# Optimization experiments

Measured on AMD Instinct MI355X. Metric: run time of the kernel, lower is better.

## Reference

```python
import jax, jax.numpy as jnp
import numpy as np

NUM_HEADS = 16

def setup_inputs() -> dict:
    key = jax.random.key(0)
    ks = jax.random.split(key, 5)
    B, T, C = 2, 2048, 1024
    s = 0.02
    return {
        "x": jax.random.normal(ks[0], (B, T, C), dtype=jnp.float32),
        "attn_w": jax.random.normal(ks[1], (3 * C, C), dtype=jnp.float32) * s,
        "attn_b": jax.random.normal(ks[2], (3 * C,), dtype=jnp.float32) * s,
        "proj_w": jax.random.normal(ks[3], (C, C), dtype=jnp.float32) * s,
        "proj_b": jax.random.normal(ks[4], (C,), dtype=jnp.float32) * s,
    }

def reference(x, attn_w, attn_b, proj_w, proj_b):
    B, T, C = x.shape
    H = NUM_HEADS
    D = C // H
    # fused QKV projection (torch Linear: x @ W^T + b)
    qkv = x @ attn_w.T + attn_b                      # [B, T, 3C]
    q, k, v = jnp.split(qkv, 3, axis=-1)             # each [B, T, C]
    # split heads -> [B, H, T, D]
    def heads(t):
        return t.reshape(B, T, H, D).transpose(0, 2, 1, 3)
    q, k, v = heads(q), heads(k), heads(v)
    scale = 1.0 / jnp.sqrt(jnp.asarray(D, dtype=x.dtype))
    scores = jnp.einsum("bhtd,bhsd->bhts", q, k) * scale   # [B, H, T, T]
    causal = jnp.tril(jnp.ones((T, T), dtype=bool))
    scores = jnp.where(causal[None, None], scores, jnp.asarray(-jnp.inf, dtype=scores.dtype))
    att = jax.nn.softmax(scores, axis=-1)
    out = jnp.einsum("bhts,bhsd->bhtd", att, v)      # [B, H, T, D]
    out = out.transpose(0, 2, 1, 3).reshape(B, T, C)
    return out @ proj_w.T + proj_b
```

## Files before the change

kernel.cpp:

```cpp
#include <hip/hip_runtime.h>
#include <hip/hip_bf16.h>

typedef __bf16 bf16_t;
typedef __bf16 bf16x4 __attribute__((ext_vector_type(4)));
typedef __bf16 bf16x8 __attribute__((ext_vector_type(8)));
typedef float f32x4 __attribute__((ext_vector_type(4)));
typedef float f32x8 __attribute__((ext_vector_type(8)));

#define MFMA16(a, b, c) __builtin_amdgcn_mfma_f32_16x16x32_bf16(a, b, c, 0, 0, 0)

#define GLOAD_LDS16(g, l)                                              \
  __builtin_amdgcn_global_load_lds(                                    \
      (const __attribute__((address_space(1))) unsigned int*)(g),      \
      (__attribute__((address_space(3))) unsigned int*)(l), 16, 0, 0)

constexpr int B = 2, T = 2048, C = 1024, H = 16, D = 64;
constexpr int NQKV = 3 * C;
constexpr int M = B * T;

__global__ __launch_bounds__(256) void cvt_kernel(
    const float* __restrict__ s0, bf16_t* __restrict__ d0, int n0,
    const float* __restrict__ s1, bf16_t* __restrict__ d1, int n1,
    const float* __restrict__ s2, bf16_t* __restrict__ d2, int n2)
{
  const float* s; bf16_t* d; int n;
  if (blockIdx.y == 0)      { s = s0; d = d0; n = n0; }
  else if (blockIdx.y == 1) { s = s1; d = d1; n = n1; }
  else                      { s = s2; d = d2; n = n2; }
  const int idx = (blockIdx.x * 256 + threadIdx.x) * 8;
  if (idx >= n) return;
  f32x8 t = *(const f32x8*)(s + idx);
  bf16x8 r;
#pragma unroll
  for (int j = 0; j < 8; ++j) r[j] = (bf16_t)t[j];
  *(bf16x8*)(d + idx) = r;
}

template<int BN, int NI>
__device__ __forceinline__ void gemm_mainloop_db(
    const bf16_t* __restrict__ A, const bf16_t* __restrict__ Wt,
    const int K, const int m0, const int n0,
    bf16_t* ldsA0, bf16_t* ldsA1, bf16_t* ldsB0, bf16_t* ldsB1,
    f32x4 acc[4][NI])
{
  const int tid  = threadIdx.x;
  const int wv   = tid >> 6;
  const int lane = tid & 63;
  const int col  = lane & 15;
  const int quad = lane >> 4;
  const int lr8  = lane >> 3;
  const int cpos = lane & 7;
  const int wm = wv >> 1, wn = wv & 1;
  constexpr int BJ = BN / 32;
  constexpr int BRW = BN / 4;

  const bf16_t* ag[4]; const bf16_t* bg[BJ];
#pragma unroll
  for (int j = 0; j < 4; ++j)
    ag[j] = A + (size_t)(m0 + wv * 32 + j * 8 + lr8) * K + (cpos ^ lr8) * 8;
#pragma unroll
  for (int j = 0; j < BJ; ++j)
    bg[j] = Wt + (size_t)(n0 + wv * BRW + j * 8 + lr8) * K + (cpos ^ lr8) * 8;

  const int xa = quad ^ (col & 7);
  const int niter = K / 64;

#pragma unroll
  for (int j = 0; j < 4; ++j)
    GLOAD_LDS16(ag[j], ldsA0 + (wv * 32 + j * 8) * 64);
#pragma unroll
  for (int j = 0; j < BJ; ++j)
    GLOAD_LDS16(bg[j], ldsB0 + (wv * BRW + j * 8) * 64);

  for (int it = 0; it < niter; ++it) {
    __syncthreads();
    const bf16_t* cA = (it & 1) ? ldsA1 : ldsA0;
    const bf16_t* cB = (it & 1) ? ldsB1 : ldsB0;
    if (it + 1 < niter) {
      bf16_t* nA = (it & 1) ? ldsA0 : ldsA1;
      bf16_t* nB = (it & 1) ? ldsB0 : ldsB1;
      const int off = (it + 1) * 64;
#pragma unroll
      for (int j = 0; j < 4; ++j)
        GLOAD_LDS16(ag[j] + off, nA + (wv * 32 + j * 8) * 64);
#pragma unroll
      for (int j = 0; j < BJ; ++j)
        GLOAD_LDS16(bg[j] + off, nB + (wv * BRW + j * 8) * 64);
    }
#pragma unroll
    for (int ks = 0; ks < 2; ++ks) {
      const int xk = (xa ^ (ks * 4)) * 8;
      bf16x8 af[4], bfr[NI];
#pragma unroll
      for (int mi = 0; mi < 4; ++mi)
        af[mi] = *(const bf16x8*)(cA + (wm * 64 + mi * 16 + col) * 64 + xk);
#pragma unroll
      for (int ni = 0; ni < NI; ++ni)
        bfr[ni] = *(const bf16x8*)(cB + (wn * (NI * 16) + ni * 16 + col) * 64 + xk);
#pragma unroll
      for (int mi = 0; mi < 4; ++mi)
#pragma unroll
        for (int ni = 0; ni < NI; ++ni)
          acc[mi][ni] = MFMA16(af[mi], bfr[ni], acc[mi][ni]);
    }
  }
}

__global__ __launch_bounds__(256) void qkv_gemm_kernel(
    const bf16_t* __restrict__ x, const bf16_t* __restrict__ w,
    const float* __restrict__ bias,
    bf16_t* __restrict__ qws, bf16_t* __restrict__ kws, bf16_t* __restrict__ vws)
{
  __shared__ __align__(16) bf16_t ldsA[2][128 * 64];
  __shared__ __align__(16) bf16_t ldsB[2][128 * 64];
  const int lane = threadIdx.x & 63;
  const int wv   = threadIdx.x >> 6;
  const int col  = lane & 15;
  const int quad = lane >> 4;
  const int wm = wv >> 1, wn = wv & 1;
  const int m0 = blockIdx.y * 128;
  const int n0 = blockIdx.x * 128;

  f32x4 acc[4][4] = {};
  gemm_mainloop_db<128, 4>(x, w, C, m0, n0,
                           ldsA[0], ldsA[1], ldsB[0], ldsB[1], acc);

  const int which = n0 >> 10;

  if (which == 2) {
    __syncthreads();
    bf16_t* vt = &ldsA[0][0] + wv * 4096;

#pragma unroll
    for (int ni = 0; ni < 4; ++ni) {
      const int n = n0 + wn * 64 + ni * 16 + col;
      const float bval = bias[n];
      const int d = n & 63;
#pragma unroll
      for (int r = 0; r < 4; ++r) {
        bf16x4 pw;
#pragma unroll
        for (int mi = 0; mi < 4; ++mi)
          pw[mi] = (bf16_t)(acc[mi][ni][r] + bval);
        const int k = 2 * quad + (r >> 1);
        const int S = d * 8 + (k ^ (d & 7));
        *(bf16x4*)(vt + S * 8 + (r & 1) * 4) = pw;
      }
    }

    const int b   = (m0 + wm * 64) >> 11;
    const int t0w = (m0 + wm * 64) & (T - 1);
    const int h   = ((n0 & (C - 1)) + wn * 64) >> 6;
    const size_t bh = (size_t)(b * H + h);
    const int lr8 = lane >> 3;
    const int c8  = lane & 7;
#pragma unroll
    for (int j = 0; j < 8; ++j) {
      const int d = j * 8 + lr8;
      bf16x8 row = *(const bf16x8*)(vt + (d * 8 + (c8 ^ (d & 7))) * 8);
      *(bf16x8*)(vws + (bh * D + d) * T + t0w + c8 * 8) = row;
    }
  } else {
#pragma unroll
    for (int ni = 0; ni < 4; ++ni) {
      const int n = n0 + wn * 64 + ni * 16 + col;
      const float bval = bias[n];
      const int c = n & (C - 1);
      const int h = c >> 6;
      const int d = c & 63;
#pragma unroll
      for (int mi = 0; mi < 4; ++mi) {
#pragma unroll
        for (int r = 0; r < 4; ++r) {
          const int m = m0 + wm * 64 + mi * 16 + quad * 4 + r;
          const int b = m >> 11;
          const int t = m & (T - 1);
          const bf16_t bv = (bf16_t)(acc[mi][ni][r] + bval);
          const size_t bh = (size_t)(b * H + h);
          if (which == 0) qws[(bh * T + t) * D + d] = bv;
          else            kws[(bh * T + t) * D + d] = bv;
        }
      }
    }
  }
}

__global__ __launch_bounds__(256) void attn_kernel(
    const bf16_t* __restrict__ qws, const bf16_t* __restrict__ kws,
    const bf16_t* __restrict__ vws, bf16_t* __restrict__ yws)
{
  const int bh = blockIdx.y;
  const int tid  = threadIdx.x;
  const int wv   = tid >> 6;
  const int lane = tid & 63;
  const int col  = lane & 15;
  const int quad = lane >> 4;

  const bf16_t* Q  = qws + (size_t)bh * T * D;
  const bf16_t* K  = kws + (size_t)bh * T * D;
  const bf16_t* Vt = vws + (size_t)bh * D * T;

  __shared__ __align__(16) bf16_t ldsK[2][64 * 64];
  __shared__ __align__(16) bf16_t ldsV[2][64 * 64];
  __shared__ __align__(16) bf16_t ldsP[4][16 * 64];
  bf16_t* ldsPw = ldsP[wv];

  const float cscale = 0.125f * 1.44269504088896340736f;

  const int xs   = col & 7;
  const int cxq  = (quad ^ xs) * 8;
  const int lr8  = lane >> 3;
  const int ksrc = (lane & 7) ^ lr8;
  const int pxor = (quad & 1) * 4;
  const int b = bh >> 4;
  const int h = bh & 15;

#pragma unroll
  for (int half = 0; half < 2; ++half) {
    const int qt = half == 0 ? (31 - (int)blockIdx.x) : (int)blockIdx.x;
    const int t0 = qt * 64;
    const int tw = t0 + 16 * wv;
    const int niter = qt + 1;

    bf16x8 qf0 = *(const bf16x8*)(Q + (size_t)(tw + col) * D + quad * 8);
    bf16x8 qf1 = *(const bf16x8*)(Q + (size_t)(tw + col) * D + 32 + quad * 8);

    f32x4 o[4] = {};
    f32x4 lp = {};

    __syncthreads();

#pragma unroll
    for (int j = 0; j < 2; ++j) {
      GLOAD_LDS16(K + (size_t)(16 * wv + j * 8 + lr8) * D + ksrc * 8,
                  ldsK[0] + (16 * wv + j * 8) * 64);
      GLOAD_LDS16(Vt + (size_t)(16 * wv + j * 8 + lr8) * T + ksrc * 8,
                  ldsV[0] + (16 * wv + j * 8) * 64);
    }

    for (int it = 0; it < niter; ++it) {
      const int s0 = it * 64;
      __syncthreads();

      if (it + 1 < niter) {
        const int sn = s0 + 64;
        bf16_t* dK = ldsK[(it + 1) & 1];
        bf16_t* dV = ldsV[(it + 1) & 1];
#pragma unroll
        for (int j = 0; j < 2; ++j) {
          GLOAD_LDS16(K + (size_t)(sn + 16 * wv + j * 8 + lr8) * D + ksrc * 8,
                      dK + (16 * wv + j * 8) * 64);
          GLOAD_LDS16(Vt + (size_t)(16 * wv + j * 8 + lr8) * T + sn + ksrc * 8,
                      dV + (16 * wv + j * 8) * 64);
        }
      }

      const bf16_t* bK = ldsK[it & 1];
      const bf16_t* bV = ldsV[it & 1];

      f32x4 sc[4];
#pragma unroll
      for (int kb = 0; kb < 4; ++kb) {
        const bf16_t* kr = bK + (kb * 16 + col) * 64;
        bf16x8 kf0 = *(const bf16x8*)(kr + cxq);
        bf16x8 kf1 = *(const bf16x8*)(kr + (cxq ^ 32));
        f32x4 a = {};
        a = MFMA16(qf0, kf0, a);
        a = MFMA16(qf1, kf1, a);
        sc[kb] = a;
      }

      const bool diag = (s0 == t0);
#pragma unroll
      for (int r = 0; r < 4; ++r) {
        const int prow = (quad * 4 + r) * 64;
        const int pxr  = pxor + r;
        bf16x4 pw;
#pragma unroll
        for (int kb = 0; kb < 4; ++kb) {
          float p = __builtin_amdgcn_exp2f(sc[kb][r] * cscale);
          if (diag && (s0 + kb * 16 + col > tw + quad * 4 + r)) p = 0.0f;
          lp[r] += p;
          pw[kb] = (bf16_t)p;
        }
        *(bf16x4*)(ldsPw + prow + (((col >> 1) ^ pxr) * 8) + (col & 1) * 4) = pw;
      }

#pragma unroll
      for (int ks = 0; ks < 2; ++ks) {
        const int xk = cxq ^ (ks * 32);
        bf16x8 pa = *(const bf16x8*)(ldsPw + col * 64 + xk);
#pragma unroll
        for (int ni = 0; ni < 4; ++ni) {
          bf16x8 vf = *(const bf16x8*)(bV + (ni * 16 + col) * 64 + xk);
          o[ni] = MFMA16(pa, vf, o[ni]);
        }
      }
    }

#pragma unroll
    for (int r = 0; r < 4; ++r) {
      float l = lp[r];
#pragma unroll
      for (int off = 1; off < 16; off <<= 1)
        l += __shfl_xor(l, off);
      const float rl = 1.0f / l;
      const int t = tw + quad * 4 + r;
#pragma unroll
      for (int ni = 0; ni < 4; ++ni) {
        const int d = ni * 16 + col;
        yws[((size_t)(b * T + t)) * C + h * D + d] = (bf16_t)(o[ni][r] * rl);
      }
    }
  }
}

__global__ __launch_bounds__(256) void proj_gemm_kernel(
    const bf16_t* __restrict__ y, const bf16_t* __restrict__ w,
    const float* __restrict__ bias, float* __restrict__ out)
{
  __shared__ __align__(16) bf16_t ldsA[2][128 * 64];
  __shared__ __align__(16) bf16_t ldsB[2][64 * 64];
  const int lane = threadIdx.x & 63;
  const int wv   = threadIdx.x >> 6;
  const int col  = lane & 15;
  const int quad = lane >> 4;
  const int wm = wv >> 1, wn = wv & 1;
  const int m0 = blockIdx.y * 128;
  const int n0 = blockIdx.x * 64;

  f32x4 acc[4][2] = {};
  gemm_mainloop_db<64, 2>(y, w, C, m0, n0,
                          ldsA[0], ldsA[1], ldsB[0], ldsB[1], acc);

#pragma unroll
  for (int ni = 0; ni < 2; ++ni) {
    const int n = n0 + wn * 32 + ni * 16 + col;
    const float bval = bias[n];
#pragma unroll
    for (int mi = 0; mi < 4; ++mi) {
#pragma unroll
      for (int r = 0; r < 4; ++r) {
        const int m = m0 + wm * 64 + mi * 16 + quad * 4 + r;
        out[(size_t)m * C + n] = acc[mi][ni][r] + bval;
      }
    }
  }
}

extern "C" void kernel_launch(void* const* d_in, const int* in_sizes, int n_in,
                              void* d_out, int out_size, void* d_ws, size_t ws_size,
                              hipStream_t stream) {
  const float* x      = (const float*)d_in[0];
  const float* attn_w = (const float*)d_in[1];
  const float* attn_b = (const float*)d_in[2];
  const float* proj_w = (const float*)d_in[3];
  const float* proj_b = (const float*)d_in[4];
  float* out = (float*)d_out;

  const size_t E = (size_t)B * H * T * D;
  char* ws = (char*)d_ws;
  bf16_t* qws = (bf16_t*)(ws);
  bf16_t* kws = (bf16_t*)(ws + 2 * E);
  bf16_t* vws = (bf16_t*)(ws + 4 * E);
  bf16_t* yws = (bf16_t*)(ws + 6 * E);
  bf16_t* xb  = (bf16_t*)(ws + 8 * E);
  bf16_t* awb = (bf16_t*)(ws + 10 * E);
  bf16_t* pwb = (bf16_t*)(ws + 11 * E + E / 2);

  const int NX = M * C, NAW = NQKV * C, NPW = C * C;
  cvt_kernel<<<dim3(NX / 2048, 3), 256, 0, stream>>>(
      x, xb, NX, attn_w, awb, NAW, proj_w, pwb, NPW);
  qkv_gemm_kernel<<<dim3(NQKV / 128, M / 128), 256, 0, stream>>>(
      xb, awb, attn_b, qws, kws, vws);
  attn_kernel<<<dim3(16, B * H), 256, 0, stream>>>(qws, kws, vws, yws);
  proj_gemm_kernel<<<dim3(C / 64, M / 128), 256, 0, stream>>>(
      yws, pwb, proj_b, out);
}
```

Before: 178.5 us.

## Share K/V tile loads across paired high and low causal query tiles

Each attention block previously processed its two paired query tiles (high and low) one after the other, streaming K/V from the start for each. Now both tiles are processed in a single pass over K/V: every loaded K/V tile is used for the high tile and, while still in range, for the low tile. This roughly halves K/V global loads and barriers per block. The grid is also flattened to 1D with bh in the low bits, so blocks for different heads interleave. The cost is twice the accumulator and Q registers, which may lower occupancy.

Result: faster. 169.2 us (-5.2%).

```diff
diff --git a/kernel.cpp b/kernel.cpp
--- a/kernel.cpp
+++ b/kernel.cpp
@@ -189,7 +189,9 @@
     const bf16_t* __restrict__ qws, const bf16_t* __restrict__ kws,
     const bf16_t* __restrict__ vws, bf16_t* __restrict__ yws)
 {
-  const int bh = blockIdx.y;
+  const int id = blockIdx.x;
+  const int bh = id & 31;
+  const int pr = id >> 5;
   const int tid  = threadIdx.x;
   const int wv   = tid >> 6;
   const int lane = tid & 63;
@@ -215,102 +217,109 @@
   const int b = bh >> 4;
   const int h = bh & 15;
 
-#pragma unroll
-  for (int half = 0; half < 2; ++half) {
-    const int qt = half == 0 ? (31 - (int)blockIdx.x) : (int)blockIdx.x;
-    const int t0 = qt * 64;
-    const int tw = t0 + 16 * wv;
-    const int niter = qt + 1;
-
-    bf16x8 qf0 = *(const bf16x8*)(Q + (size_t)(tw + col) * D + quad * 8);
-    bf16x8 qf1 = *(const bf16x8*)(Q + (size_t)(tw + col) * D + 32 + quad * 8);
-
-    f32x4 o[4] = {};
-    f32x4 lp = {};
-
+  const int qt_h = 31 - pr, qt_l = pr;
+  const int t0h = qt_h * 64, t0l = qt_l * 64;
+  const int twh = t0h + 16 * wv, twl = t0l + 16 * wv;
+  const int niter = qt_h + 1;
+
+  bf16x8 qfh0 = *(const bf16x8*)(Q + (size_t)(twh + col) * D + quad * 8);
+  bf16x8 qfh1 = *(const bf16x8*)(Q + (size_t)(twh + col) * D + 32 + quad * 8);
+  bf16x8 qfl0 = *(const bf16x8*)(Q + (size_t)(twl + col) * D + quad * 8);
+  bf16x8 qfl1 = *(const bf16x8*)(Q + (size_t)(twl + col) * D + 32 + quad * 8);
+
+  f32x4 oh[4] = {}, ol[4] = {};
+  f32x4 lph = {}, lpl = {};
+
+  auto compute_tile = [&](const bf16_t* bK, const bf16_t* bV, int s0, int tw,
+                          int t0, bf16x8 qf0, bf16x8 qf1,
+                          f32x4 (&o)[4], f32x4& lp) {
+    f32x4 sc[4];
+#pragma unroll
+    for (int kb = 0; kb < 4; ++kb) {
+      const bf16_t* kr = bK + (kb * 16 + col) * 64;
+      bf16x8 kf0 = *(const bf16x8*)(kr + cxq);
+      bf16x8 kf1 = *(const bf16x8*)(kr + (cxq ^ 32));
+      f32x4 a = {};
+      a = MFMA16(qf0, kf0, a);
+      a = MFMA16(qf1, kf1, a);
+      sc[kb] = a;
+    }
+    const bool diag = (s0 == t0);
+#pragma unroll
+    for (int r = 0; r < 4; ++r) {
+      const int prow = (quad * 4 + r) * 64;
+      const int pxr  = pxor + r;
+      bf16x4 pw;
+#pragma unroll
+      for (int kb = 0; kb < 4; ++kb) {
+        float p = __builtin_amdgcn_exp2f(sc[kb][r] * cscale);
+        if (diag && (s0 + kb * 16 + col > tw + quad * 4 + r)) p = 0.0f;
+        lp[r] += p;
+        pw[kb] = (bf16_t)p;
+      }
+      *(bf16x4*)(ldsPw + prow + (((col >> 1) ^ pxr) * 8) + (col & 1) * 4) = pw;
+    }
+#pragma unroll
+    for (int ks = 0; ks < 2; ++ks) {
+      const int xk = cxq ^ (ks * 32);
+      bf16x8 pa = *(const bf16x8*)(ldsPw + col * 64 + xk);
+#pragma unroll
+      for (int ni = 0; ni < 4; ++ni) {
+        bf16x8 vf = *(const bf16x8*)(bV + (ni * 16 + col) * 64 + xk);
+        o[ni] = MFMA16(pa, vf, o[ni]);
+      }
+    }
+  };
+
+#pragma unroll
+  for (int j = 0; j < 2; ++j) {
+    GLOAD_LDS16(K + (size_t)(16 * wv + j * 8 + lr8) * D + ksrc * 8,
+                ldsK[0] + (16 * wv + j * 8) * 64);
+    GLOAD_LDS16(Vt + (size_t)(16 * wv + j * 8 + lr8) * T + ksrc * 8,
+                ldsV[0] + (16 * wv + j * 8) * 64);
+  }
+
+  for (int it = 0; it < niter; ++it) {
+    const int s0 = it * 64;
     __syncthreads();
 
-#pragma unroll
-    for (int j = 0; j < 2; ++j) {
-      GLOAD_LDS16(K + (size_t)(16 * wv + j * 8 + lr8) * D + ksrc * 8,
-                  ldsK[0] + (16 * wv + j * 8) * 64);
-      GLOAD_LDS16(Vt + (size_t)(16 * wv + j * 8 + lr8) * T + ksrc * 8,
-                  ldsV[0] + (16 * wv + j * 8) * 64);
-    }
-
-    for (int it = 0; it < niter; ++it) {
-      const int s0 = it * 64;
-      __syncthreads();
-
-      if (it + 1 < niter) {
-        const int sn = s0 + 64;
-        bf16_t* dK = ldsK[(it + 1) & 1];
-        bf16_t* dV = ldsV[(it + 1) & 1];
-#pragma unroll
-        for (int j = 0; j < 2; ++j) {
-          GLOAD_LDS16(K + (size_t)(sn + 16 * wv + j * 8 + lr8) * D + ksrc * 8,
-                      dK + (16 * wv + j * 8) * 64);
-          GLOAD_LDS16(Vt + (size_t)(16 * wv + j * 8 + lr8) * T + sn + ksrc * 8,
-                      dV + (16 * wv + j * 8) * 64);
-        }
-      }
-
-      const bf16_t* bK = ldsK[it & 1];
-      const bf16_t* bV = ldsV[it & 1];
-
-      f32x4 sc[4];
-#pragma unroll
-      for (int kb = 0; kb < 4; ++kb) {
-        const bf16_t* kr = bK + (kb * 16 + col) * 64;
-        bf16x8 kf0 = *(const bf16x8*)(kr + cxq);
-        bf16x8 kf1 = *(const bf16x8*)(kr + (cxq ^ 32));
-        f32x4 a = {};
-        a = MFMA16(qf0, kf0, a);
-        a = MFMA16(qf1, kf1, a);
-        sc[kb] = a;
-      }
-
-      const bool diag = (s0 == t0);
-#pragma unroll
-      for (int r = 0; r < 4; ++r) {
-        const int prow = (quad * 4 + r) * 64;
-        const int pxr  = pxor + r;
-        bf16x4 pw;
-#pragma unroll
-        for (int kb = 0; kb < 4; ++kb) {
-          float p = __builtin_amdgcn_exp2f(sc[kb][r] * cscale);
-          if (diag && (s0 + kb * 16 + col > tw + quad * 4 + r)) p = 0.0f;
-          lp[r] += p;
-          pw[kb] = (bf16_t)p;
-        }
-        *(bf16x4*)(ldsPw + prow + (((col >> 1) ^ pxr) * 8) + (col & 1) * 4) = pw;
-      }
-
-#pragma unroll
-      for (int ks = 0; ks < 2; ++ks) {
-        const int xk = cxq ^ (ks * 32);
-        bf16x8 pa = *(const bf16x8*)(ldsPw + col * 64 + xk);
-#pragma unroll
-        for (int ni = 0; ni < 4; ++ni) {
-          bf16x8 vf = *(const bf16x8*)(bV + (ni * 16 + col) * 64 + xk);
-          o[ni] = MFMA16(pa, vf, o[ni]);
-        }
-      }
-    }
-
-#pragma unroll
-    for (int r = 0; r < 4; ++r) {
-      float l = lp[r];
-#pragma unroll
-      for (int off = 1; off < 16; off <<= 1)
-        l += __shfl_xor(l, off);
-      const float rl = 1.0f / l;
-      const int t = tw + quad * 4 + r;
-#pragma unroll
-      for (int ni = 0; ni < 4; ++ni) {
-        const int d = ni * 16 + col;
-        yws[((size_t)(b * T + t)) * C + h * D + d] = (bf16_t)(o[ni][r] * rl);
-      }
+    if (it + 1 < niter) {
+      const int sn = s0 + 64;
+      bf16_t* dK = ldsK[(it + 1) & 1];
+      bf16_t* dV = ldsV[(it + 1) & 1];
+#pragma unroll
+      for (int j = 0; j < 2; ++j) {
+        GLOAD_LDS16(K + (size_t)(sn + 16 * wv + j * 8 + lr8) * D + ksrc * 8,
+                    dK + (16 * wv + j * 8) * 64);
+        GLOAD_LDS16(Vt + (size_t)(16 * wv + j * 8 + lr8) * T + sn + ksrc * 8,
+                    dV + (16 * wv + j * 8) * 64);
+      }
+    }
+
+    const bf16_t* bK = ldsK[it & 1];
+    const bf16_t* bV = ldsV[it & 1];
+
+    compute_tile(bK, bV, s0, twh, t0h, qfh0, qfh1, oh, lph);
+    if (s0 <= t0l)
+      compute_tile(bK, bV, s0, twl, t0l, qfl0, qfl1, ol, lpl);
+  }
+
+#pragma unroll
+  for (int r = 0; r < 4; ++r) {
+    float l0 = lph[r], l1 = lpl[r];
+#pragma unroll
+    for (int off = 1; off < 16; off <<= 1) {
+      l0 += __shfl_xor(l0, off);
+      l1 += __shfl_xor(l1, off);
+    }
+    const float rl0 = 1.0f / l0, rl1 = 1.0f / l1;
+    const int th = twh + quad * 4 + r;
+    const int tl = twl + quad * 4 + r;
+#pragma unroll
+    for (int ni = 0; ni < 4; ++ni) {
+      const int d = ni * 16 + col;
+      yws[((size_t)(b * T + th)) * C + h * D + d] = (bf16_t)(oh[ni][r] * rl0);
+      yws[((size_t)(b * T + tl)) * C + h * D + d] = (bf16_t)(ol[ni][r] * rl1);
     }
   }
 }
@@ -373,7 +382,7 @@
       x, xb, NX, attn_w, awb, NAW, proj_w, pwb, NPW);
   qkv_gemm_kernel<<<dim3(NQKV / 128, M / 128), 256, 0, stream>>>(
       xb, awb, attn_b, qws, kws, vws);
-  attn_kernel<<<dim3(16, B * H), 256, 0, stream>>>(qws, kws, vws, yws);
+  attn_kernel<<<512, 256, 0, stream>>>(qws, kws, vws, yws);
   proj_gemm_kernel<<<dim3(C / 64, M / 128), 256, 0, stream>>>(
       yws, pwb, proj_b, out);
 }
```
